# Optimization experiments

Hardware: AMD Instinct MI355X
Metric: run time of the kernel (lower is better)

Reference implementation:

```python
import math
import jax, jax.numpy as jnp
import numpy as np

N, D, K = 8192, 256, 32


def setup_inputs() -> dict:
    key = jax.random.key(0)
    kx, kw, kb = jax.random.split(key, 3)
    x = jax.random.normal(kx, (N, D), dtype=jnp.float32)
    # params per _init_weights: w ~ N(1, 0.01), b ~ N(0, 0.01)
    w = 1.0 + 0.01 * jax.random.normal(kw, (K, D), dtype=jnp.float32)
    b = 0.01 * jax.random.normal(kb, (K, D), dtype=jnp.float32)
    return {"x": x, "w": w, "b": b}


def reference(x, w, b):
    # x: (N, D); w, b: (K, D)
    y1 = w[None, :, :] * (x[:, None, :] + b[None, :, :])        # (N, K, D)
    y2 = y1 * y1                                                 # (N, K, D)
    y4 = -0.5 * jnp.sum(y2, axis=-1)                             # (N, K)
    gamma = jax.nn.softmax(y4, axis=-1)                          # (N, K)
    y6 = (y2 - 1.0) * (1.0 / math.sqrt(2.0))                     # (N, K, D)
    g = gamma[:, :, None]                                        # (N, K, 1)
    n, kk, d = y1.shape
    sigma_part = (g * y6).reshape(n, kk * d)                     # (N, K*D)
    mu_part = (g * y1).reshape(n, kk * d)                        # (N, K*D)
    phi_patches = jnp.concatenate([sigma_part, mu_part], axis=-1)
    return jnp.mean(phi_patches, axis=0)                         # (2*K*D,)
```

## Files before the change

### kernel.cpp

```cpp
#include <hip/hip_runtime.h>
#include <math.h>

#define Nn 8192
#define Dd 256
#define Kk 32

#define P_OFF   0
#define P2_OFF  4194304
#define SP_OFF  4325376

__global__ __launch_bounds__(1024) void fused_kernel(const float* __restrict__ x,
                                                     const float* __restrict__ w,
                                                     const float* __restrict__ b,
                                                     float* __restrict__ ws) {
    __shared__ __align__(16) float4 uS4[64 * 33];
    __shared__ __align__(16) float4 vS4[64 * 33];
    __shared__ __align__(16) float  gS[1024];

    float* P  = ws + P_OFF;
    float* Sp = ws + SP_OFF;
    int tid = threadIdx.x;
    int blk = blockIdx.x;

    {
        const float4* w4 = (const float4*)w;
        const float4* b4 = (const float4*)b;
        #pragma unroll
        for (int i = 0; i < 2; ++i) {
            int e4 = tid + i * 1024;
            int k  = e4 >> 6;
            int d4 = e4 & 63;
            float4 wv = w4[e4];
            float4 bv = b4[e4];
            float4 vv = {wv.x * bv.x, wv.y * bv.y, wv.z * bv.z, wv.w * bv.w};
            uS4[d4 * 33 + k] = wv;
            vS4[d4 * 33 + k] = vv;
        }
    }
    __syncthreads();

    {
        int lane = tid & 63;
        int wave = tid >> 6;
        int k = lane & 31;
        int h = lane >> 5;
        int r0 = wave * 2;
        size_t rowbase = (size_t)blk * 32 + r0;

        const float4* xr0 = (const float4*)(x + (rowbase + 0) * Dd);
        const float4* xr1 = (const float4*)(x + (rowbase + 1) * Dd);

        float4 a0 = {0.f, 0.f, 0.f, 0.f}, a1 = a0;

        #pragma unroll 8
        for (int i = 0; i < 32; ++i) {
            int ii = h * 32 + i;
            float4 u  = uS4[ii * 33 + k];
            float4 v  = vS4[ii * 33 + k];
            float4 x0 = xr0[ii];
            float4 x1 = xr1[ii];
            float y;
            y = fmaf(u.x, x0.x, v.x); a0.x = fmaf(y, y, a0.x);
            y = fmaf(u.y, x0.y, v.y); a0.y = fmaf(y, y, a0.y);
            y = fmaf(u.z, x0.z, v.z); a0.z = fmaf(y, y, a0.z);
            y = fmaf(u.w, x0.w, v.w); a0.w = fmaf(y, y, a0.w);
            y = fmaf(u.x, x1.x, v.x); a1.x = fmaf(y, y, a1.x);
            y = fmaf(u.y, x1.y, v.y); a1.y = fmaf(y, y, a1.y);
            y = fmaf(u.z, x1.z, v.z); a1.z = fmaf(y, y, a1.z);
            y = fmaf(u.w, x1.w, v.w); a1.w = fmaf(y, y, a1.w);
        }

        float s0 = (a0.x + a0.y) + (a0.z + a0.w);
        float s1 = (a1.x + a1.y) + (a1.z + a1.w);
        s0 += __shfl_xor(s0, 32);
        s1 += __shfl_xor(s1, 32);
        float y40 = -0.5f * s0, y41 = -0.5f * s1;

        float m0 = y40, m1 = y41;
        #pragma unroll
        for (int o = 16; o >= 1; o >>= 1) {
            m0 = fmaxf(m0, __shfl_xor(m0, o));
            m1 = fmaxf(m1, __shfl_xor(m1, o));
        }
        float e0 = __expf(y40 - m0), e1 = __expf(y41 - m1);
        float t0 = e0, t1 = e1;
        #pragma unroll
        for (int o = 16; o >= 1; o >>= 1) {
            t0 += __shfl_xor(t0, o);
            t1 += __shfl_xor(t1, o);
        }
        if (h == 0) {
            gS[(r0 + 0) * 32 + k] = e0 / t0;
            gS[(r0 + 1) * 32 + k] = e1 / t1;
        }
    }
    __syncthreads();

    if (tid < 32) {
        float s0 = 0.f, s1 = 0.f, s2 = 0.f, s3 = 0.f;
        #pragma unroll
        for (int r = 0; r < 32; r += 4) {
            s0 += gS[(r + 0) * 32 + tid];
            s1 += gS[(r + 1) * 32 + tid];
            s2 += gS[(r + 2) * 32 + tid];
            s3 += gS[(r + 3) * 32 + tid];
        }
        Sp[blk * 32 + tid] = (s0 + s1) + (s2 + s3);
    }

    {
        int kq = tid >> 8;
        int d  = tid & 255;
        const float* xcol = x + ((size_t)blk * 32) * Dd + d;
        const float4* gS4 = (const float4*)gS;

        float aG[8], aH[8];
        #pragma unroll
        for (int j = 0; j < 8; ++j) { aG[j] = 0.f; aH[j] = 0.f; }

        #pragma unroll 4
        for (int r = 0; r < 32; ++r) {
            float xv = xcol[(size_t)r * Dd];
            float xx = xv * xv;
            #pragma unroll
            for (int q = 0; q < 2; ++q) {
                float4 gv = gS4[r * 8 + kq * 2 + q];
                aG[4*q+0] = fmaf(gv.x, xv, aG[4*q+0]); aH[4*q+0] = fmaf(gv.x, xx, aH[4*q+0]);
                aG[4*q+1] = fmaf(gv.y, xv, aG[4*q+1]); aH[4*q+1] = fmaf(gv.y, xx, aH[4*q+1]);
                aG[4*q+2] = fmaf(gv.z, xv, aG[4*q+2]); aH[4*q+2] = fmaf(gv.z, xx, aH[4*q+2]);
                aG[4*q+3] = fmaf(gv.w, xv, aG[4*q+3]); aH[4*q+3] = fmaf(gv.w, xx, aH[4*q+3]);
            }
        }

        #pragma unroll
        for (int j = 0; j < 8; ++j) {
            int k = kq * 8 + j;
            P[((size_t)(k * 2 + 0) * 256 + blk) * 256 + d] = aG[j];
            P[((size_t)(k * 2 + 1) * 256 + blk) * 256 + d] = aH[j];
        }
    }
}

__global__ __launch_bounds__(256) void red1_kernel(float* __restrict__ ws) {
    const float* P = ws + P_OFF;
    float* P2 = ws + P2_OFF;
    int tid = threadIdx.x;
    int k  = blockIdx.x >> 4;
    int gh = (blockIdx.x >> 3) & 1;
    int c  = blockIdx.x & 7;

    const float* p = P + ((size_t)(k * 2 + gh) * 256 + c * 32) * 256 + tid;
    float s0 = 0.f, s1 = 0.f, s2 = 0.f, s3 = 0.f;
    #pragma unroll
    for (int i = 0; i < 32; i += 4) {
        s0 += p[(size_t)(i + 0) * 256];
        s1 += p[(size_t)(i + 1) * 256];
        s2 += p[(size_t)(i + 2) * 256];
        s3 += p[(size_t)(i + 3) * 256];
    }
    P2[((size_t)(k * 2 + gh) * 8 + c) * 256 + tid] = (s0 + s1) + (s2 + s3);
}

__global__ __launch_bounds__(256) void red2_kernel(const float* __restrict__ w,
                                                   const float* __restrict__ b,
                                                   const float* __restrict__ ws,
                                                   float* __restrict__ out) {
    const float* P2 = ws + P2_OFF;
    const float* Sp = ws + SP_OFF;
    __shared__ float sred[4];
    int k = blockIdx.x, d = threadIdx.x;

    float sv_part = Sp[d * 32 + k];
    #pragma unroll
    for (int o = 32; o >= 1; o >>= 1) sv_part += __shfl_xor(sv_part, o);
    if ((d & 63) == 0) sred[d >> 6] = sv_part;
    __syncthreads();
    float sv = (sred[0] + sred[1]) + (sred[2] + sred[3]);

    const float* pg = P2 + (size_t)(k * 2 + 0) * 8 * 256 + d;
    const float* ph = P2 + (size_t)(k * 2 + 1) * 8 * 256 + d;
    float Gv = 0.f, Hv = 0.f;
    #pragma unroll
    for (int c = 0; c < 8; ++c) {
        Gv += pg[c * 256];
        Hv += ph[c * 256];
    }

    int idx = k * Dd + d;
    float wv = w[idx], bv = b[idx];
    const float invN = 1.0f / 8192.0f;
    const float c2 = 0.70710678118654752440f * invN;
    float mu = wv * (Gv + bv * sv) * invN;
    float w2 = wv * wv;
    float sg = (w2 * (Hv + 2.0f * bv * Gv + bv * bv * sv) - sv) * c2;
    out[idx] = sg;
    out[Kk * Dd + idx] = mu;
}

extern "C" void kernel_launch(void* const* d_in, const int* in_sizes, int n_in,
                              void* d_out, int out_size, void* d_ws, size_t ws_size,
                              hipStream_t stream) {
    const float* x = (const float*)d_in[0];
    const float* w = (const float*)d_in[1];
    const float* b = (const float*)d_in[2];
    float* out = (float*)d_out;
    float* ws = (float*)d_ws;

    hipLaunchKernelGGL(fused_kernel, dim3(256), dim3(1024), 0, stream, x, w, b, ws);
    hipLaunchKernelGGL(red1_kernel,  dim3(512), dim3(256),  0, stream, ws);
    hipLaunchKernelGGL(red2_kernel,  dim3(32),  dim3(256),  0, stream, w, b, ws, out);
}
```

Baseline: 83.45 us.

## Register-block four rows per thread in distance pass and stage gamma through global

The squared-distance phase now gives each thread four rows over half of D, instead of two rows over the full D. Each u/v value loaded from LDS is therefore reused across more rows. Partial sums from the two D halves are combined through a new shared buffer, which costs an extra barrier. Gamma is also written to a global workspace region and read back from there in the accumulation phase instead of from LDS, which may offload LDS traffic but adds global memory traffic and relies on block-level visibility of global writes.

```diff
diff --git a/kernel.cpp b/kernel.cpp
--- a/kernel.cpp
+++ b/kernel.cpp
@@ -8,6 +8,7 @@
 #define P_OFF   0
 #define P2_OFF  4194304
 #define SP_OFF  4325376
+#define G_OFF   4333568
 
 __global__ __launch_bounds__(1024) void fused_kernel(const float* __restrict__ x,
                                                      const float* __restrict__ w,
@@ -15,10 +16,12 @@
                                                      float* __restrict__ ws) {
     __shared__ __align__(16) float4 uS4[64 * 33];
     __shared__ __align__(16) float4 vS4[64 * 33];
-    __shared__ __align__(16) float  gS[1024];
+    __shared__ float hS[2 * 8 * 4 * 32];
+    __shared__ float gS[1024];
 
     float* P  = ws + P_OFF;
     float* Sp = ws + SP_OFF;
+    float* G  = ws + G_OFF;
     int tid = threadIdx.x;
     int blk = blockIdx.x;
 
@@ -42,23 +45,26 @@
     {
         int lane = tid & 63;
         int wave = tid >> 6;
-        int k = lane & 31;
-        int h = lane >> 5;
-        int r0 = wave * 2;
-        size_t rowbase = (size_t)blk * 32 + r0;
-
-        const float4* xr0 = (const float4*)(x + (rowbase + 0) * Dd);
-        const float4* xr1 = (const float4*)(x + (rowbase + 1) * Dd);
-
-        float4 a0 = {0.f, 0.f, 0.f, 0.f}, a1 = a0;
-
-        #pragma unroll 8
-        for (int i = 0; i < 32; ++i) {
-            int ii = h * 32 + i;
-            float4 u  = uS4[ii * 33 + k];
-            float4 v  = vS4[ii * 33 + k];
-            float4 x0 = xr0[ii];
-            float4 x1 = xr1[ii];
+        int k  = lane & 31;
+        int s  = lane >> 5;
+        int h  = wave & 1;
+        int rg = wave >> 1;
+        int d4base = h * 32 + s * 16;
+
+        const float4* xr = (const float4*)x + ((size_t)blk * 32 + rg * 4) * 64 + d4base;
+        const float4* uP = uS4 + d4base * 33 + k;
+        const float4* vP = vS4 + d4base * 33 + k;
+
+        float4 a0 = {0.f, 0.f, 0.f, 0.f}, a1 = a0, a2 = a0, a3 = a0;
+
+        #pragma unroll 2
+        for (int i = 0; i < 16; ++i) {
+            float4 u  = uP[i * 33];
+            float4 v  = vP[i * 33];
+            float4 x0 = xr[i];
+            float4 x1 = xr[i + 64];
+            float4 x2 = xr[i + 128];
+            float4 x3 = xr[i + 192];
             float y;
             y = fmaf(u.x, x0.x, v.x); a0.x = fmaf(y, y, a0.x);
             y = fmaf(u.y, x0.y, v.y); a0.y = fmaf(y, y, a0.y);
@@ -68,13 +74,46 @@
             y = fmaf(u.y, x1.y, v.y); a1.y = fmaf(y, y, a1.y);
             y = fmaf(u.z, x1.z, v.z); a1.z = fmaf(y, y, a1.z);
             y = fmaf(u.w, x1.w, v.w); a1.w = fmaf(y, y, a1.w);
+            y = fmaf(u.x, x2.x, v.x); a2.x = fmaf(y, y, a2.x);
+            y = fmaf(u.y, x2.y, v.y); a2.y = fmaf(y, y, a2.y);
+            y = fmaf(u.z, x2.z, v.z); a2.z = fmaf(y, y, a2.z);
+            y = fmaf(u.w, x2.w, v.w); a2.w = fmaf(y, y, a2.w);
+            y = fmaf(u.x, x3.x, v.x); a3.x = fmaf(y, y, a3.x);
+            y = fmaf(u.y, x3.y, v.y); a3.y = fmaf(y, y, a3.y);
+            y = fmaf(u.z, x3.z, v.z); a3.z = fmaf(y, y, a3.z);
+            y = fmaf(u.w, x3.w, v.w); a3.w = fmaf(y, y, a3.w);
         }
 
         float s0 = (a0.x + a0.y) + (a0.z + a0.w);
         float s1 = (a1.x + a1.y) + (a1.z + a1.w);
+        float s2 = (a2.x + a2.y) + (a2.z + a2.w);
+        float s3 = (a3.x + a3.y) + (a3.z + a3.w);
         s0 += __shfl_xor(s0, 32);
         s1 += __shfl_xor(s1, 32);
-        float y40 = -0.5f * s0, y41 = -0.5f * s1;
+        s2 += __shfl_xor(s2, 32);
+        s3 += __shfl_xor(s3, 32);
+        if (s == 0) {
+            int base = (h * 8 + rg) * 128 + k;
+            hS[base +  0] = s0;
+            hS[base + 32] = s1;
+            hS[base + 64] = s2;
+            hS[base + 96] = s3;
+        }
+    }
+    __syncthreads();
+
+    {
+        int lane = tid & 63;
+        int wave = tid >> 6;
+        int k  = lane & 31;
+        int h2 = lane >> 5;
+        int r0 = wave * 2;
+        int r1 = r0 + 1;
+
+        float y40 = -0.5f * (hS[(r0 >> 2) * 128 + (r0 & 3) * 32 + k]
+                           + hS[1024 + (r0 >> 2) * 128 + (r0 & 3) * 32 + k]);
+        float y41 = -0.5f * (hS[(r1 >> 2) * 128 + (r1 & 3) * 32 + k]
+                           + hS[1024 + (r1 >> 2) * 128 + (r1 & 3) * 32 + k]);
 
         float m0 = y40, m1 = y41;
         #pragma unroll
@@ -89,9 +128,12 @@
             t0 += __shfl_xor(t0, o);
             t1 += __shfl_xor(t1, o);
         }
-        if (h == 0) {
-            gS[(r0 + 0) * 32 + k] = e0 / t0;
-            gS[(r0 + 1) * 32 + k] = e1 / t1;
+        if (h2 == 0) {
+            float g0 = e0 / t0, g1 = e1 / t1;
+            gS[r0 * 32 + k] = g0;
+            gS[r1 * 32 + k] = g1;
+            G[(size_t)blk * 1024 + r0 * 32 + k] = g0;
+            G[(size_t)blk * 1024 + r1 * 32 + k] = g1;
         }
     }
     __syncthreads();
@@ -112,7 +154,7 @@
         int kq = tid >> 8;
         int d  = tid & 255;
         const float* xcol = x + ((size_t)blk * 32) * Dd + d;
-        const float4* gS4 = (const float4*)gS;
+        const float4* g4 = (const float4*)(G + (size_t)blk * 1024);
 
         float aG[8], aH[8];
         #pragma unroll
@@ -124,7 +166,7 @@
             float xx = xv * xv;
             #pragma unroll
             for (int q = 0; q < 2; ++q) {
-                float4 gv = gS4[r * 8 + kq * 2 + q];
+                float4 gv = g4[r * 8 + kq * 2 + q];
                 aG[4*q+0] = fmaf(gv.x, xv, aG[4*q+0]); aH[4*q+0] = fmaf(gv.x, xx, aH[4*q+0]);
                 aG[4*q+1] = fmaf(gv.y, xv, aG[4*q+1]); aH[4*q+1] = fmaf(gv.y, xx, aH[4*q+1]);
                 aG[4*q+2] = fmaf(gv.z, xv, aG[4*q+2]); aH[4*q+2] = fmaf(gv.z, xx, aH[4*q+2]);
```

Result: slower. 88.71 us (+6.3%).
